# Kernel tuning notes

Hardware: AMD Instinct MI355X
Metric: run time of the kernel (lower is better)

Reference implementation:

```python
import jax, jax.numpy as jnp
import numpy as np


def _l2n(v, eps=1e-12):
    return v / (jnp.linalg.norm(v) + eps)


def _sn(W, u):
    # Spectral normalization with one power-iteration step.
    # W: [Cin, Cout] (1x1 conv kernel flattened), u: [Cin] persistent vector.
    v = _l2n(W.T @ u)            # [Cout]
    u_new = _l2n(W @ v)          # [Cin]
    v = jax.lax.stop_gradient(v)
    u_new = jax.lax.stop_gradient(u_new)
    sigma = u_new @ (W @ v)      # scalar, grads flow through W only
    return W / sigma


def _conv1x1(x, W, b, u):
    # x: [B,H,W,Cin], spectrally-normalized 1x1 conv == GEMM over channels
    return jnp.einsum('bhwc,cd->bhwd', x, _sn(W, u)) + b


def setup_inputs() -> dict:
    key = jax.random.key(0)
    ks = jax.random.split(key, 14)
    B, H, W, C = 8, 64, 64, 256
    Cq = C // 8  # 32
    s = lambda fan_in: 1.0 / np.sqrt(fan_in)
    return {
        'x':  jax.random.normal(ks[0], (B, H, W, C), jnp.float32),
        'Wf': jax.random.normal(ks[1], (C, Cq), jnp.float32) * s(C),
        'bf': jnp.zeros((Cq,), jnp.float32),
        'uf': jax.random.normal(ks[2], (C,), jnp.float32),
        'Wg': jax.random.normal(ks[3], (C, Cq), jnp.float32) * s(C),
        'bg': jnp.zeros((Cq,), jnp.float32),
        'ug': jax.random.normal(ks[4], (C,), jnp.float32),
        'Wh': jax.random.normal(ks[5], (C, C), jnp.float32) * s(C),
        'bh': jnp.zeros((C,), jnp.float32),
        'uh': jax.random.normal(ks[6], (C,), jnp.float32),
        'Wc': jax.random.normal(ks[7], (C, C), jnp.float32) * s(C),
        'bc': jnp.zeros((C,), jnp.float32),
        'uc': jax.random.normal(ks[8], (C,), jnp.float32),
        'gamma': jnp.float32(0.7),  # nonzero so attention branch contributes
    }


def reference(x, Wf, bf, uf, Wg, bg, ug, Wh, bh, uh, Wc, bc, uc, gamma):
    B, H, W, C = x.shape
    N = H * W
    flat = lambda t: t.reshape(B, N, t.shape[-1])
    f = flat(_conv1x1(x, Wf, bf, uf))   # [B,N,C/8] keys
    g = flat(_conv1x1(x, Wg, bg, ug))   # [B,N,C/8] queries
    h = flat(_conv1x1(x, Wh, bh, uh))   # [B,N,C]   values
    s = jnp.einsum('bqd,bkd->bqk', g, f)          # [B,N,N]
    beta = jax.nn.softmax(s, axis=-1)
    o = jnp.einsum('bqk,bkc->bqc', beta, h)       # [B,N,C]
    o = o.reshape(B, H, W, C)
    o = _conv1x1(o, Wc, bc, uc)
    return gamma * o + x
```

## Files before the change

### kernel.cpp

```cpp
#include <hip/hip_runtime.h>

typedef unsigned short ushort_t;
typedef __attribute__((ext_vector_type(8))) __bf16 bf16x8;
typedef __attribute__((ext_vector_type(4))) float f32x4;
typedef __attribute__((ext_vector_type(4))) ushort_t ushort4_t;

__device__ inline ushort_t f2bf(float f){
  __bf16 h = (__bf16)f;
  union { __bf16 h; ushort_t u; } v; v.h = h;
  return v.u;
}

__device__ inline f32x4 mfma16(bf16x8 a, bf16x8 b, f32x4 c){
  return __builtin_amdgcn_mfma_f32_16x16x32_bf16(a, b, c, 0, 0, 0);
}

#define GLDS16(gsrc, ldst) \
  __builtin_amdgcn_global_load_lds((const __attribute__((address_space(1))) unsigned int*)(gsrc), \
                                   (__attribute__((address_space(3))) unsigned int*)(ldst), 16, 0, 0)

__global__ void sigma_kernel(const float* __restrict__ Wf, const float* __restrict__ uf,
                             const float* __restrict__ Wg, const float* __restrict__ ug,
                             const float* __restrict__ Wh, const float* __restrict__ uh,
                             const float* __restrict__ Wc, const float* __restrict__ uc,
                             float* __restrict__ inv_sigma){
  int w = blockIdx.x, t = threadIdx.x;
  const float *W, *u; int Cout;
  if      (w == 0){ W = Wf; u = uf; Cout = 32; }
  else if (w == 1){ W = Wg; u = ug; Cout = 32; }
  else if (w == 2){ W = Wh; u = uh; Cout = 256; }
  else            { W = Wc; u = uc; Cout = 256; }
  __shared__ float su[256], sv[256], red[256];
  su[t] = u[t];
  __syncthreads();
  float v = 0.f;
  if (t < Cout){
    for (int i = 0; i < 256; ++i) v += W[i*Cout + t] * su[i];
  }
  red[t] = (t < Cout) ? v*v : 0.f;
  __syncthreads();
  for (int s = 128; s > 0; s >>= 1){ if (t < s) red[t] += red[t+s]; __syncthreads(); }
  float nv = sqrtf(red[0]) + 1e-12f;
  __syncthreads();
  if (t < Cout) sv[t] = v / nv;
  __syncthreads();
  float wv = 0.f;
  for (int d = 0; d < Cout; ++d) wv += W[t*Cout + d] * sv[d];
  __syncthreads();
  red[t] = wv * wv;
  __syncthreads();
  for (int s = 128; s > 0; s >>= 1){ if (t < s) red[t] += red[t+s]; __syncthreads(); }
  if (t == 0){
    float ss2 = red[0];
    float sig = ss2 / (sqrtf(ss2) + 1e-12f);
    inv_sigma[w] = 1.0f / sig;
  }
}

__global__ void prep_weights(const float* __restrict__ Wf, const float* __restrict__ Wg,
                             const float* __restrict__ Wh, const float* __restrict__ Wc,
                             const float* __restrict__ inv_sigma,
                             ushort_t* __restrict__ WallT, ushort_t* __restrict__ WcT){
  int idx = blockIdx.x * 256 + threadIdx.x;
  if (idx < 81920){
    int c = idx >> 8, k = idx & 255;
    float val, is;
    if (c < 32)      { val = Wf[k*32  + c      ]; is = inv_sigma[0]; }
    else if (c < 64) { val = Wg[k*32  + (c-32) ]; is = inv_sigma[1]; }
    else             { val = Wh[k*256 + (c-64) ]; is = inv_sigma[2]; }
    WallT[idx] = f2bf(val * is);
  } else {
    int j = idx - 81920; int c = j >> 8, k = j & 255;
    WcT[j] = f2bf(Wc[k*256 + c] * inv_sigma[3]);
  }
}

__global__ __launch_bounds__(256) void fgh_kernel(
    const float* __restrict__ x, const ushort_t* __restrict__ WallT,
    const float* __restrict__ bf, const float* __restrict__ bg, const float* __restrict__ bh,
    ushort_t* __restrict__ fO, ushort_t* __restrict__ gO, ushort_t* __restrict__ hT){
  __shared__ __attribute__((aligned(16))) char ldsX[4][16384];
  int t = threadIdx.x;
  int wv = t >> 6, l = t & 63, lrow = l & 15, lgrp = l >> 4;
  long r0 = (long)blockIdx.x * 64 + wv * 16;
  char* ldsW = ldsX[wv];
#pragma unroll
  for (int rloc = 0; rloc < 16; ++rloc){
    const char* src = (const char*)(x + (r0 + rloc)*256)
                    + ((l*16) ^ ((rloc & 7) << 4));
    GLDS16(src, ldsW + rloc*1024);
  }
  asm volatile("s_waitcnt vmcnt(0)" ::: "memory");
  const char* xrow = ldsW + lrow*1024;
  int swzX = (lrow & 7) << 4;
  f32x4 acc[20];
#pragma unroll
  for (int i = 0; i < 20; ++i) acc[i] = f32x4{0.f,0.f,0.f,0.f};
#pragma unroll
  for (int ks = 0; ks < 8; ++ks){
    int bb = ks*128 + lgrp*32;
    f32x4 xa = *(const f32x4*)(xrow + ( bb       ^ swzX));
    f32x4 xb = *(const f32x4*)(xrow + ((bb + 16) ^ swzX));
    union { __bf16 h[8]; bf16x8 v; } A;
#pragma unroll
    for (int j = 0; j < 4; ++j){ A.h[j] = (__bf16)xa[j]; A.h[4+j] = (__bf16)xb[j]; }
    int kk = ks*32 + lgrp*8;
#pragma unroll
    for (int ct = 0; ct < 20; ++ct){
      bf16x8 bbv = *(const bf16x8*)(WallT + (ct*16 + lrow)*256 + kk);
      acc[ct] = mfma16(A.v, bbv, acc[ct]);
    }
  }
#pragma unroll
  for (int ct = 0; ct < 20; ++ct){
    int col = ct*16 + lrow;
    long rowb = r0 + lgrp*4;
    if (col < 32){
      float bv = bf[col];
#pragma unroll
      for (int rg = 0; rg < 4; ++rg) fO[(rowb+rg)*32 + col] = f2bf(acc[ct][rg] + bv);
    } else if (col < 64){
      float bv = bg[col-32];
#pragma unroll
      for (int rg = 0; rg < 4; ++rg)
        gO[(rowb+rg)*32 + (col-32)] = f2bf((acc[ct][rg] + bv) * 1.44269504f);
    } else {
      int hc = col - 64;
      float bv = bh[hc];
      long bb2 = rowb >> 12, n = rowb & 4095;
      ushort4_t pk;
#pragma unroll
      for (int rg = 0; rg < 4; ++rg) pk[rg] = f2bf(acc[ct][rg] + bv);
      *(ushort4_t*)(hT + (bb2*256 + hc)*4096 + n) = pk;
    }
  }
}

__global__ __launch_bounds__(256, 4) void attn_kernel(
    const ushort_t* __restrict__ fI, const ushort_t* __restrict__ gI,
    const ushort_t* __restrict__ hT,
    ushort_t* __restrict__ oP, float* __restrict__ mP, float* __restrict__ liP){
  __shared__ ushort_t ldsV[256*64];
  __shared__ ushort_t ldsP[4][16*64];
  int bid = blockIdx.x, t = threadIdx.x;
  int b = bid & 7, rest = bid >> 3, qt = rest >> 1, kh = rest & 1;
  int wv = t >> 6, l = t & 63, lrow = l & 15, lgrp = l >> 4;
  int q0 = qt*64 + wv*16;
  long key_base = (long)kh * 2048;
  bf16x8 qa = *(const bf16x8*)(gI + ((long)b*4096 + q0 + lrow)*32 + lgrp*8);
  const ushort_t* hB = hT + (long)b*256*4096;
  const ushort_t* kp = fI + (long)b*4096*32 + key_base*32 + lrow*32 + lgrp*8;
  const ushort_t* vsrc = hB + (long)(wv*64 + (l>>3))*4096 + key_base
                            + (((l & 7) ^ (l >> 3)) << 3);
  ushort_t* vdst = ldsV + wv*4096;
  f32x4 o[16];
#pragma unroll
  for (int i = 0; i < 16; ++i) o[i] = f32x4{0.f,0.f,0.f,0.f};
  float m = -1e30f, li = 0.f;
  int swzR = (lrow & 7) << 3;
  ushort_t* Pw = ldsP[wv];
  for (int kt = 0; kt < 32; ++kt){
    __syncthreads();
    bf16x8 kb0 = *(const bf16x8*)(kp);
    bf16x8 kb1 = *(const bf16x8*)(kp + 512);
    bf16x8 kb2 = *(const bf16x8*)(kp + 1024);
    bf16x8 kb3 = *(const bf16x8*)(kp + 1536);
    kp += 2048;
    const ushort_t* vs = vsrc + kt*64;
#pragma unroll
    for (int i = 0; i < 8; ++i)
      GLDS16(vs + i*32768, vdst + i*512);
    f32x4 s0 = mfma16(kb0, qa, f32x4{0.f,0.f,0.f,0.f});
    f32x4 s1 = mfma16(kb1, qa, f32x4{0.f,0.f,0.f,0.f});
    f32x4 s2 = mfma16(kb2, qa, f32x4{0.f,0.f,0.f,0.f});
    f32x4 s3 = mfma16(kb3, qa, f32x4{0.f,0.f,0.f,0.f});
    float tm = fmaxf(fmaxf(fmaxf(s0[0], s0[1]), fmaxf(s0[2], s0[3])),
               fmaxf(fmaxf(s1[0], s1[1]), fmaxf(s1[2], s1[3])));
    tm = fmaxf(tm, fmaxf(fmaxf(fmaxf(s2[0], s2[1]), fmaxf(s2[2], s2[3])),
                         fmaxf(fmaxf(s3[0], s3[1]), fmaxf(s3[2], s3[3]))));
    tm = fmaxf(tm, __shfl_xor(tm, 16));
    tm = fmaxf(tm, __shfl_xor(tm, 32));
    if (__any(tm > m + 8.f)){
      float mn = fmaxf(m, tm);
      float sc = exp2f(m - mn);
      m = mn; li *= sc;
      float sc_o[4];
#pragma unroll
      for (int rg = 0; rg < 4; ++rg)
        sc_o[rg] = __shfl(sc, (l & 48) | ((l >> 2) & 12) | rg);
#pragma unroll
      for (int ct = 0; ct < 16; ++ct)
#pragma unroll
        for (int rg = 0; rg < 4; ++rg) o[ct][rg] *= sc_o[rg];
    }
#pragma unroll
    for (int st = 0; st < 4; ++st){
      f32x4 sv = (st == 0) ? s0 : (st == 1) ? s1 : (st == 2) ? s2 : s3;
      float p0 = exp2f(sv[0] - m);
      float p1 = exp2f(sv[1] - m);
      float p2 = exp2f(sv[2] - m);
      float p3 = exp2f(sv[3] - m);
      li += (p0 + p1) + (p2 + p3);
      ushort4_t pk;
      pk[0] = f2bf(p0); pk[1] = f2bf(p1); pk[2] = f2bf(p2); pk[3] = f2bf(p3);
      *(ushort4_t*)(Pw + (((lrow << 6) + (st << 4) + (lgrp << 2)) ^ swzR)) = pk;
    }
    asm volatile("s_waitcnt lgkmcnt(0)" ::: "memory");
    __builtin_amdgcn_sched_barrier(0);
    bf16x8 pa0 = *(const bf16x8*)(Pw + (((lrow << 6) + (lgrp << 3))      ^ swzR));
    bf16x8 pa1 = *(const bf16x8*)(Pw + (((lrow << 6) + (lgrp << 3) + 32) ^ swzR));
    asm volatile("s_waitcnt vmcnt(0)" ::: "memory");
    __syncthreads();
    __builtin_amdgcn_s_setprio(1);
#pragma unroll
    for (int ct = 0; ct < 16; ++ct){
      int base = (ct*16 + lrow) << 6;
      bf16x8 b0 = *(const bf16x8*)(ldsV + base + (((lgrp << 3))      ^ swzR));
      bf16x8 b1 = *(const bf16x8*)(ldsV + base + (((lgrp << 3) + 32) ^ swzR));
      o[ct] = mfma16(pa0, b0, o[ct]);
      o[ct] = mfma16(pa1, b1, o[ct]);
    }
    __builtin_amdgcn_s_setprio(0);
  }
  li += __shfl_xor(li, 16);
  li += __shfl_xor(li, 32);
  long rbase = (long)b*4096 + q0;
  ushort_t* Ob = oP + ((long)kh*32768 + rbase)*256;
#pragma unroll
  for (int ct = 0; ct < 16; ++ct){
    int col = ct*16 + lrow;
#pragma unroll
    for (int rg = 0; rg < 4; ++rg){
      int row = lgrp*4 + rg;
      Ob[(long)row*256 + col] = f2bf(o[ct][rg]);
    }
  }
  if (l < 16){
    mP [kh*32768 + rbase + lrow] = m;
    liP[kh*32768 + rbase + lrow] = li;
  }
}

__global__ __launch_bounds__(256) void out_kernel(
    const ushort_t* __restrict__ oP, const float* __restrict__ mP,
    const float* __restrict__ liP, const ushort_t* __restrict__ WcT,
    const float* __restrict__ bc, const float* __restrict__ x,
    const float* __restrict__ gamma, float* __restrict__ out){
  __shared__ __attribute__((aligned(16))) char ldsO[4][16384];
  int t = threadIdx.x;
  int wv = t >> 6, l = t & 63, lrow = l & 15, lgrp = l >> 4;
  long r0 = (long)blockIdx.x * 64 + wv * 16;
  char* ldsW = ldsO[wv];
#pragma unroll
  for (int i = 0; i < 8; ++i){
    int rloc = 2*i + (l >> 5);
    int soff = ((l & 31)*16) ^ ((rloc & 7) << 4);
    GLDS16((const char*)(oP + (r0 + rloc)*256) + soff,            ldsW + i*1024);
    GLDS16((const char*)(oP + (32768L + r0 + rloc)*256) + soff,   ldsW + 8192 + i*1024);
  }
  long r = r0 + lrow;
  float m1 = mP[r],  m2 = mP[32768 + r];
  float li1 = liP[r], li2 = liP[32768 + r];
  float mm  = fmaxf(m1, m2);
  float sc1 = exp2f(m1 - mm), sc2 = exp2f(m2 - mm);
  float inv = 1.0f / (li1*sc1 + li2*sc2);
  float w1 = sc1 * inv, w2 = sc2 * inv;
  asm volatile("s_waitcnt vmcnt(0)" ::: "memory");
  const char* orow = ldsW + lrow*512;
  int swzO = (lrow & 7) << 4;
  f32x4 acc[16];
#pragma unroll
  for (int i = 0; i < 16; ++i) acc[i] = f32x4{0.f,0.f,0.f,0.f};
#pragma unroll
  for (int ks = 0; ks < 8; ++ks){
    int bb = (ks*64 + lgrp*16) ^ swzO;
    bf16x8 a1 = *(const bf16x8*)(orow + bb);
    bf16x8 a2 = *(const bf16x8*)(orow + 8192 + bb);
    union { __bf16 h[8]; bf16x8 v; } A;
#pragma unroll
    for (int j = 0; j < 8; ++j)
      A.h[j] = (__bf16)((float)a1[j]*w1 + (float)a2[j]*w2);
    int kk = ks*32 + lgrp*8;
#pragma unroll
    for (int ct = 0; ct < 16; ++ct){
      bf16x8 bbv = *(const bf16x8*)(WcT + (ct*16 + lrow)*256 + kk);
      acc[ct] = mfma16(A.v, bbv, acc[ct]);
    }
  }
  float gm = gamma[0];
#pragma unroll
  for (int ct = 0; ct < 16; ++ct){
    int col = ct*16 + lrow;
    float bv = bc[col];
#pragma unroll
    for (int rg = 0; rg < 4; ++rg){
      long row = r0 + lgrp*4 + rg;
      out[row*256 + col] = gm*(acc[ct][rg] + bv) + x[row*256 + col];
    }
  }
}

extern "C" void kernel_launch(void* const* d_in, const int* in_sizes, int n_in,
                              void* d_out, int out_size, void* d_ws, size_t ws_size,
                              hipStream_t stream){
  (void)in_sizes; (void)n_in; (void)out_size; (void)ws_size;
  const float* x  = (const float*)d_in[0];
  const float* Wf = (const float*)d_in[1];
  const float* bf = (const float*)d_in[2];
  const float* uf = (const float*)d_in[3];
  const float* Wg = (const float*)d_in[4];
  const float* bg = (const float*)d_in[5];
  const float* ug = (const float*)d_in[6];
  const float* Wh = (const float*)d_in[7];
  const float* bh = (const float*)d_in[8];
  const float* uh = (const float*)d_in[9];
  const float* Wc = (const float*)d_in[10];
  const float* bc = (const float*)d_in[11];
  const float* uc = (const float*)d_in[12];
  const float* gamma = (const float*)d_in[13];
  float* out = (float*)d_out;

  char* w = (char*)d_ws;
  float*    inv_sigma = (float*)w;
  ushort_t* WallT = (ushort_t*)(w + 256);
  ushort_t* WcT   = (ushort_t*)(w + 164096);
  ushort_t* fW    = (ushort_t*)(w + 295168);
  ushort_t* gW    = (ushort_t*)(w + 2392320);
  ushort_t* hTW   = (ushort_t*)(w + 4489472);
  ushort_t* oPW   = (ushort_t*)(w + 21266688);
  float*    mPW   = (float*)   (w + 54821120);
  float*    liPW  = (float*)   (w + 55083264);

  hipLaunchKernelGGL(sigma_kernel, dim3(4),    dim3(256), 0, stream,
                     Wf, uf, Wg, ug, Wh, uh, Wc, uc, inv_sigma);
  hipLaunchKernelGGL(prep_weights, dim3(576),  dim3(256), 0, stream,
                     Wf, Wg, Wh, Wc, inv_sigma, WallT, WcT);
  hipLaunchKernelGGL(fgh_kernel,   dim3(512),  dim3(256), 0, stream,
                     x, WallT, bf, bg, bh, fW, gW, hTW);
  hipLaunchKernelGGL(attn_kernel,  dim3(1024), dim3(256), 0, stream,
                     fW, gW, hTW, oPW, mPW, liPW);
  hipLaunchKernelGGL(out_kernel,   dim3(512),  dim3(256), 0, stream,
                     oPW, mPW, liPW, WcT, bc, x, gamma, out);
}
```

Baseline: 219.4 us.

## Process two query tiles per wave and keep P in registers via V permutation

Each wave now handles 32 query rows instead of 16, so every K and V tile loaded into LDS is reused across twice as many queries, and the grid is halved. The V layout written by the fgh kernel is permuted within 64-key blocks so the softmax probabilities from the QK MFMA output can feed the PV MFMA straight from registers, removing the LDS round-trip for P. Output stores are vectorized. The cost is roughly doubled accumulator registers and occupancy lowered to 2 blocks per SIMD-set, with fewer blocks to fill the device.

```diff
diff --git a/kernel.cpp b/kernel.cpp
--- a/kernel.cpp
+++ b/kernel.cpp
@@ -128,37 +128,40 @@
       int hc = col - 64;
       float bv = bh[hc];
       long bb2 = rowb >> 12, n = rowb & 4095;
+      int k6 = (int)(n & 63);
+      int s6 = (k6 & 32) | (((k6 >> 2) & 3) << 3) | (((k6 >> 4) & 1) << 2) | (k6 & 3);
+      long pos = (n & ~63L) | (long)s6;
       ushort4_t pk;
 #pragma unroll
       for (int rg = 0; rg < 4; ++rg) pk[rg] = f2bf(acc[ct][rg] + bv);
-      *(ushort4_t*)(hT + (bb2*256 + hc)*4096 + n) = pk;
-    }
-  }
-}
-
-__global__ __launch_bounds__(256, 4) void attn_kernel(
+      *(ushort4_t*)(hT + (bb2*256 + hc)*4096 + pos) = pk;
+    }
+  }
+}
+
+__global__ __launch_bounds__(256, 2) void attn_kernel(
     const ushort_t* __restrict__ fI, const ushort_t* __restrict__ gI,
     const ushort_t* __restrict__ hT,
     ushort_t* __restrict__ oP, float* __restrict__ mP, float* __restrict__ liP){
   __shared__ ushort_t ldsV[256*64];
-  __shared__ ushort_t ldsP[4][16*64];
   int bid = blockIdx.x, t = threadIdx.x;
   int b = bid & 7, rest = bid >> 3, qt = rest >> 1, kh = rest & 1;
   int wv = t >> 6, l = t & 63, lrow = l & 15, lgrp = l >> 4;
-  int q0 = qt*64 + wv*16;
+  int q0 = qt*128 + wv*32;
   long key_base = (long)kh * 2048;
-  bf16x8 qa = *(const bf16x8*)(gI + ((long)b*4096 + q0 + lrow)*32 + lgrp*8);
+  const ushort_t* gB = gI + ((long)b*4096 + q0)*32;
+  bf16x8 qa0 = *(const bf16x8*)(gB + lrow*32 + lgrp*8);
+  bf16x8 qa1 = *(const bf16x8*)(gB + (16 + lrow)*32 + lgrp*8);
   const ushort_t* hB = hT + (long)b*256*4096;
   const ushort_t* kp = fI + (long)b*4096*32 + key_base*32 + lrow*32 + lgrp*8;
   const ushort_t* vsrc = hB + (long)(wv*64 + (l>>3))*4096 + key_base
                             + (((l & 7) ^ (l >> 3)) << 3);
   ushort_t* vdst = ldsV + wv*4096;
-  f32x4 o[16];
-#pragma unroll
-  for (int i = 0; i < 16; ++i) o[i] = f32x4{0.f,0.f,0.f,0.f};
-  float m = -1e30f, li = 0.f;
+  f32x4 o0[16], o1[16];
+#pragma unroll
+  for (int i = 0; i < 16; ++i){ o0[i] = f32x4{0.f,0.f,0.f,0.f}; o1[i] = f32x4{0.f,0.f,0.f,0.f}; }
+  float m0 = -1e30f, m1 = -1e30f, li0 = 0.f, li1 = 0.f;
   int swzR = (lrow & 7) << 3;
-  ushort_t* Pw = ldsP[wv];
   for (int kt = 0; kt < 32; ++kt){
     __syncthreads();
     bf16x8 kb0 = *(const bf16x8*)(kp);
@@ -170,74 +173,77 @@
 #pragma unroll
     for (int i = 0; i < 8; ++i)
       GLDS16(vs + i*32768, vdst + i*512);
-    f32x4 s0 = mfma16(kb0, qa, f32x4{0.f,0.f,0.f,0.f});
-    f32x4 s1 = mfma16(kb1, qa, f32x4{0.f,0.f,0.f,0.f});
-    f32x4 s2 = mfma16(kb2, qa, f32x4{0.f,0.f,0.f,0.f});
-    f32x4 s3 = mfma16(kb3, qa, f32x4{0.f,0.f,0.f,0.f});
-    float tm = fmaxf(fmaxf(fmaxf(s0[0], s0[1]), fmaxf(s0[2], s0[3])),
-               fmaxf(fmaxf(s1[0], s1[1]), fmaxf(s1[2], s1[3])));
-    tm = fmaxf(tm, fmaxf(fmaxf(fmaxf(s2[0], s2[1]), fmaxf(s2[2], s2[3])),
-                         fmaxf(fmaxf(s3[0], s3[1]), fmaxf(s3[2], s3[3]))));
-    tm = fmaxf(tm, __shfl_xor(tm, 16));
-    tm = fmaxf(tm, __shfl_xor(tm, 32));
-    if (__any(tm > m + 8.f)){
-      float mn = fmaxf(m, tm);
-      float sc = exp2f(m - mn);
-      m = mn; li *= sc;
-      float sc_o[4];
-#pragma unroll
-      for (int rg = 0; rg < 4; ++rg)
-        sc_o[rg] = __shfl(sc, (l & 48) | ((l >> 2) & 12) | rg);
+    f32x4 s00 = mfma16(kb0, qa0, f32x4{0.f,0.f,0.f,0.f});
+    f32x4 s01 = mfma16(kb1, qa0, f32x4{0.f,0.f,0.f,0.f});
+    f32x4 s02 = mfma16(kb2, qa0, f32x4{0.f,0.f,0.f,0.f});
+    f32x4 s03 = mfma16(kb3, qa0, f32x4{0.f,0.f,0.f,0.f});
+    f32x4 s10 = mfma16(kb0, qa1, f32x4{0.f,0.f,0.f,0.f});
+    f32x4 s11 = mfma16(kb1, qa1, f32x4{0.f,0.f,0.f,0.f});
+    f32x4 s12 = mfma16(kb2, qa1, f32x4{0.f,0.f,0.f,0.f});
+    f32x4 s13 = mfma16(kb3, qa1, f32x4{0.f,0.f,0.f,0.f});
+    float tm0 = -1e30f, tm1 = -1e30f;
+#pragma unroll
+    for (int rg = 0; rg < 4; ++rg){
+      tm0 = fmaxf(tm0, fmaxf(fmaxf(s00[rg], s01[rg]), fmaxf(s02[rg], s03[rg])));
+      tm1 = fmaxf(tm1, fmaxf(fmaxf(s10[rg], s11[rg]), fmaxf(s12[rg], s13[rg])));
+    }
+    tm0 = fmaxf(tm0, __shfl_xor(tm0, 16)); tm0 = fmaxf(tm0, __shfl_xor(tm0, 32));
+    tm1 = fmaxf(tm1, __shfl_xor(tm1, 16)); tm1 = fmaxf(tm1, __shfl_xor(tm1, 32));
+    if (__any((tm0 > m0 + 8.f) || (tm1 > m1 + 8.f))){
+      float mn0 = fmaxf(m0, tm0), mn1 = fmaxf(m1, tm1);
+      float sc0 = exp2f(m0 - mn0), sc1 = exp2f(m1 - mn1);
+      m0 = mn0; m1 = mn1; li0 *= sc0; li1 *= sc1;
 #pragma unroll
       for (int ct = 0; ct < 16; ++ct)
 #pragma unroll
-        for (int rg = 0; rg < 4; ++rg) o[ct][rg] *= sc_o[rg];
-    }
-#pragma unroll
-    for (int st = 0; st < 4; ++st){
-      f32x4 sv = (st == 0) ? s0 : (st == 1) ? s1 : (st == 2) ? s2 : s3;
-      float p0 = exp2f(sv[0] - m);
-      float p1 = exp2f(sv[1] - m);
-      float p2 = exp2f(sv[2] - m);
-      float p3 = exp2f(sv[3] - m);
-      li += (p0 + p1) + (p2 + p3);
-      ushort4_t pk;
-      pk[0] = f2bf(p0); pk[1] = f2bf(p1); pk[2] = f2bf(p2); pk[3] = f2bf(p3);
-      *(ushort4_t*)(Pw + (((lrow << 6) + (st << 4) + (lgrp << 2)) ^ swzR)) = pk;
-    }
-    asm volatile("s_waitcnt lgkmcnt(0)" ::: "memory");
-    __builtin_amdgcn_sched_barrier(0);
-    bf16x8 pa0 = *(const bf16x8*)(Pw + (((lrow << 6) + (lgrp << 3))      ^ swzR));
-    bf16x8 pa1 = *(const bf16x8*)(Pw + (((lrow << 6) + (lgrp << 3) + 32) ^ swzR));
+        for (int rg = 0; rg < 4; ++rg){ o0[ct][rg] *= sc0; o1[ct][rg] *= sc1; }
+    }
+    union { __bf16 h[8]; bf16x8 v; } pf00, pf01, pf10, pf11;
+#pragma unroll
+    for (int rg = 0; rg < 4; ++rg){
+      float a0 = exp2f(s00[rg] - m0), a1 = exp2f(s01[rg] - m0);
+      float a2 = exp2f(s02[rg] - m0), a3 = exp2f(s03[rg] - m0);
+      li0 += (a0 + a1) + (a2 + a3);
+      pf00.h[rg] = (__bf16)a0; pf00.h[4+rg] = (__bf16)a1;
+      pf01.h[rg] = (__bf16)a2; pf01.h[4+rg] = (__bf16)a3;
+      float c0 = exp2f(s10[rg] - m1), c1 = exp2f(s11[rg] - m1);
+      float c2 = exp2f(s12[rg] - m1), c3 = exp2f(s13[rg] - m1);
+      li1 += (c0 + c1) + (c2 + c3);
+      pf10.h[rg] = (__bf16)c0; pf10.h[4+rg] = (__bf16)c1;
+      pf11.h[rg] = (__bf16)c2; pf11.h[4+rg] = (__bf16)c3;
+    }
     asm volatile("s_waitcnt vmcnt(0)" ::: "memory");
     __syncthreads();
     __builtin_amdgcn_s_setprio(1);
 #pragma unroll
     for (int ct = 0; ct < 16; ++ct){
       int base = (ct*16 + lrow) << 6;
-      bf16x8 b0 = *(const bf16x8*)(ldsV + base + (((lgrp << 3))      ^ swzR));
-      bf16x8 b1 = *(const bf16x8*)(ldsV + base + (((lgrp << 3) + 32) ^ swzR));
-      o[ct] = mfma16(pa0, b0, o[ct]);
-      o[ct] = mfma16(pa1, b1, o[ct]);
+      bf16x8 vb0 = *(const bf16x8*)(ldsV + base + (( (lgrp << 3))      ^ swzR));
+      bf16x8 vb1 = *(const bf16x8*)(ldsV + base + ((32 + (lgrp << 3)) ^ swzR));
+      o0[ct] = mfma16(vb0, pf00.v, o0[ct]);
+      o0[ct] = mfma16(vb1, pf01.v, o0[ct]);
+      o1[ct] = mfma16(vb0, pf10.v, o1[ct]);
+      o1[ct] = mfma16(vb1, pf11.v, o1[ct]);
     }
     __builtin_amdgcn_s_setprio(0);
   }
-  li += __shfl_xor(li, 16);
-  li += __shfl_xor(li, 32);
+  li0 += __shfl_xor(li0, 16); li0 += __shfl_xor(li0, 32);
+  li1 += __shfl_xor(li1, 16); li1 += __shfl_xor(li1, 32);
   long rbase = (long)b*4096 + q0;
   ushort_t* Ob = oP + ((long)kh*32768 + rbase)*256;
 #pragma unroll
   for (int ct = 0; ct < 16; ++ct){
-    int col = ct*16 + lrow;
-#pragma unroll
-    for (int rg = 0; rg < 4; ++rg){
-      int row = lgrp*4 + rg;
-      Ob[(long)row*256 + col] = f2bf(o[ct][rg]);
-    }
+    ushort4_t pk0, pk1;
+#pragma unroll
+    for (int rg = 0; rg < 4; ++rg){ pk0[rg] = f2bf(o0[ct][rg]); pk1[rg] = f2bf(o1[ct][rg]); }
+    *(ushort4_t*)(Ob + (long)lrow*256      + ct*16 + lgrp*4) = pk0;
+    *(ushort4_t*)(Ob + (long)(16+lrow)*256 + ct*16 + lgrp*4) = pk1;
   }
   if (l < 16){
-    mP [kh*32768 + rbase + lrow] = m;
-    liP[kh*32768 + rbase + lrow] = li;
+    mP [kh*32768 + rbase + lrow]      = m0;
+    liP[kh*32768 + rbase + lrow]      = li0;
+    mP [kh*32768 + rbase + 16 + lrow] = m1;
+    liP[kh*32768 + rbase + 16 + lrow] = li1;
   }
 }
 
@@ -337,7 +343,7 @@
                      Wf, Wg, Wh, Wc, inv_sigma, WallT, WcT);
   hipLaunchKernelGGL(fgh_kernel,   dim3(512),  dim3(256), 0, stream,
                      x, WallT, bf, bg, bh, fW, gW, hTW);
-  hipLaunchKernelGGL(attn_kernel,  dim3(1024), dim3(256), 0, stream,
+  hipLaunchKernelGGL(attn_kernel,  dim3(512),  dim3(256), 0, stream,
                      fW, gW, hTW, oPW, mPW, liPW);
   hipLaunchKernelGGL(out_kernel,   dim3(512),  dim3(256), 0, stream,
                      oPW, mPW, liPW, WcT, bc, x, gamma, out);
```

After: 206.2 us. 1.06x faster.

## Keep softmax probabilities in registers by permuting V layout and transposing PV MFMA

Applied to the files above, without the earlier changes.

The projection kernel now writes the transposed value tensor with keys permuted inside each 64-key block, so the attention kernel can feed exp'd scores straight from the S MFMA output registers as the B operand of a transposed PV MFMA. This removes the per-tile LDS round trip for P (store, wait, reload) and the per-row scale shuffles, since each lane now owns one query column. The row max shuffle moves inside the rare rescale branch, and output stores become vectorized 4-wide. It relies on the key permutation matching the MFMA register layout exactly; any mismatch corrupts results.

```diff
diff --git a/kernel.cpp b/kernel.cpp
--- a/kernel.cpp
+++ b/kernel.cpp
@@ -128,10 +128,13 @@
       int hc = col - 64;
       float bv = bh[hc];
       long bb2 = rowb >> 12, n = rowb & 4095;
+      int k6 = (int)(n & 63);
+      int s6 = (k6 & 32) | (((k6 >> 2) & 3) << 3) | (((k6 >> 4) & 1) << 2) | (k6 & 3);
+      long pos = (n & ~63L) | (long)s6;
       ushort4_t pk;
 #pragma unroll
       for (int rg = 0; rg < 4; ++rg) pk[rg] = f2bf(acc[ct][rg] + bv);
-      *(ushort4_t*)(hT + (bb2*256 + hc)*4096 + n) = pk;
+      *(ushort4_t*)(hT + (bb2*256 + hc)*4096 + pos) = pk;
     }
   }
 }
@@ -141,11 +144,10 @@
     const ushort_t* __restrict__ hT,
     ushort_t* __restrict__ oP, float* __restrict__ mP, float* __restrict__ liP){
   __shared__ ushort_t ldsV[256*64];
-  __shared__ ushort_t ldsP[4][16*64];
   int bid = blockIdx.x, t = threadIdx.x;
-  int b = bid & 7, rest = bid >> 3, qt = rest >> 1, kh = rest & 1;
+  int b = bid & 7, rest = bid >> 3, qg = rest >> 1, kh = rest & 1;
   int wv = t >> 6, l = t & 63, lrow = l & 15, lgrp = l >> 4;
-  int q0 = qt*64 + wv*16;
+  int q0 = qg*64 + wv*16;
   long key_base = (long)kh * 2048;
   bf16x8 qa = *(const bf16x8*)(gI + ((long)b*4096 + q0 + lrow)*32 + lgrp*8);
   const ushort_t* hB = hT + (long)b*256*4096;
@@ -158,7 +160,6 @@
   for (int i = 0; i < 16; ++i) o[i] = f32x4{0.f,0.f,0.f,0.f};
   float m = -1e30f, li = 0.f;
   int swzR = (lrow & 7) << 3;
-  ushort_t* Pw = ldsP[wv];
   for (int kt = 0; kt < 32; ++kt){
     __syncthreads();
     bf16x8 kb0 = *(const bf16x8*)(kp);
@@ -170,55 +171,45 @@
 #pragma unroll
     for (int i = 0; i < 8; ++i)
       GLDS16(vs + i*32768, vdst + i*512);
-    f32x4 s0 = mfma16(kb0, qa, f32x4{0.f,0.f,0.f,0.f});
-    f32x4 s1 = mfma16(kb1, qa, f32x4{0.f,0.f,0.f,0.f});
-    f32x4 s2 = mfma16(kb2, qa, f32x4{0.f,0.f,0.f,0.f});
-    f32x4 s3 = mfma16(kb3, qa, f32x4{0.f,0.f,0.f,0.f});
-    float tm = fmaxf(fmaxf(fmaxf(s0[0], s0[1]), fmaxf(s0[2], s0[3])),
-               fmaxf(fmaxf(s1[0], s1[1]), fmaxf(s1[2], s1[3])));
-    tm = fmaxf(tm, fmaxf(fmaxf(fmaxf(s2[0], s2[1]), fmaxf(s2[2], s2[3])),
-                         fmaxf(fmaxf(s3[0], s3[1]), fmaxf(s3[2], s3[3]))));
-    tm = fmaxf(tm, __shfl_xor(tm, 16));
-    tm = fmaxf(tm, __shfl_xor(tm, 32));
+    f32x4 z = f32x4{0.f,0.f,0.f,0.f};
+    f32x4 s0 = mfma16(kb0, qa, z);
+    f32x4 s1 = mfma16(kb1, qa, z);
+    f32x4 s2 = mfma16(kb2, qa, z);
+    f32x4 s3 = mfma16(kb3, qa, z);
+    float tm = -1e30f;
+#pragma unroll
+    for (int rg = 0; rg < 4; ++rg)
+      tm = fmaxf(tm, fmaxf(fmaxf(s0[rg], s1[rg]), fmaxf(s2[rg], s3[rg])));
     if (__any(tm > m + 8.f)){
+      tm = fmaxf(tm, __shfl_xor(tm, 16));
+      tm = fmaxf(tm, __shfl_xor(tm, 32));
       float mn = fmaxf(m, tm);
       float sc = exp2f(m - mn);
       m = mn; li *= sc;
-      float sc_o[4];
-#pragma unroll
-      for (int rg = 0; rg < 4; ++rg)
-        sc_o[rg] = __shfl(sc, (l & 48) | ((l >> 2) & 12) | rg);
 #pragma unroll
       for (int ct = 0; ct < 16; ++ct)
 #pragma unroll
-        for (int rg = 0; rg < 4; ++rg) o[ct][rg] *= sc_o[rg];
-    }
-#pragma unroll
-    for (int st = 0; st < 4; ++st){
-      f32x4 sv = (st == 0) ? s0 : (st == 1) ? s1 : (st == 2) ? s2 : s3;
-      float p0 = exp2f(sv[0] - m);
-      float p1 = exp2f(sv[1] - m);
-      float p2 = exp2f(sv[2] - m);
-      float p3 = exp2f(sv[3] - m);
-      li += (p0 + p1) + (p2 + p3);
-      ushort4_t pk;
-      pk[0] = f2bf(p0); pk[1] = f2bf(p1); pk[2] = f2bf(p2); pk[3] = f2bf(p3);
-      *(ushort4_t*)(Pw + (((lrow << 6) + (st << 4) + (lgrp << 2)) ^ swzR)) = pk;
-    }
-    asm volatile("s_waitcnt lgkmcnt(0)" ::: "memory");
-    __builtin_amdgcn_sched_barrier(0);
-    bf16x8 pa0 = *(const bf16x8*)(Pw + (((lrow << 6) + (lgrp << 3))      ^ swzR));
-    bf16x8 pa1 = *(const bf16x8*)(Pw + (((lrow << 6) + (lgrp << 3) + 32) ^ swzR));
+        for (int rg = 0; rg < 4; ++rg) o[ct][rg] *= sc;
+    }
+    union { __bf16 h[8]; bf16x8 v; } pf0, pf1;
+#pragma unroll
+    for (int rg = 0; rg < 4; ++rg){
+      float a0 = exp2f(s0[rg] - m), a1 = exp2f(s1[rg] - m);
+      float a2 = exp2f(s2[rg] - m), a3 = exp2f(s3[rg] - m);
+      li += (a0 + a1) + (a2 + a3);
+      pf0.h[rg] = (__bf16)a0; pf0.h[4+rg] = (__bf16)a1;
+      pf1.h[rg] = (__bf16)a2; pf1.h[4+rg] = (__bf16)a3;
+    }
     asm volatile("s_waitcnt vmcnt(0)" ::: "memory");
     __syncthreads();
     __builtin_amdgcn_s_setprio(1);
 #pragma unroll
     for (int ct = 0; ct < 16; ++ct){
       int base = (ct*16 + lrow) << 6;
-      bf16x8 b0 = *(const bf16x8*)(ldsV + base + (((lgrp << 3))      ^ swzR));
-      bf16x8 b1 = *(const bf16x8*)(ldsV + base + (((lgrp << 3) + 32) ^ swzR));
-      o[ct] = mfma16(pa0, b0, o[ct]);
-      o[ct] = mfma16(pa1, b1, o[ct]);
+      bf16x8 vb0 = *(const bf16x8*)(ldsV + base + (( (lgrp << 3))      ^ swzR));
+      bf16x8 vb1 = *(const bf16x8*)(ldsV + base + ((32 + (lgrp << 3)) ^ swzR));
+      o[ct] = mfma16(vb0, pf0.v, o[ct]);
+      o[ct] = mfma16(vb1, pf1.v, o[ct]);
     }
     __builtin_amdgcn_s_setprio(0);
   }
@@ -228,12 +219,10 @@
   ushort_t* Ob = oP + ((long)kh*32768 + rbase)*256;
 #pragma unroll
   for (int ct = 0; ct < 16; ++ct){
-    int col = ct*16 + lrow;
-#pragma unroll
-    for (int rg = 0; rg < 4; ++rg){
-      int row = lgrp*4 + rg;
-      Ob[(long)row*256 + col] = f2bf(o[ct][rg]);
-    }
+    ushort4_t pk;
+#pragma unroll
+    for (int rg = 0; rg < 4; ++rg) pk[rg] = f2bf(o[ct][rg]);
+    *(ushort4_t*)(Ob + (long)lrow*256 + ct*16 + lgrp*4) = pk;
   }
   if (l < 16){
     mP [kh*32768 + rbase + lrow] = m;
```

New measurement: 216.0 us. Within noise of the previous version (-1.5%).
